# Optimization experiments

Measured on AMD Instinct MI355X. Metric: run time of the kernel, lower is better.

Reference implementation:

```python
import jax, jax.numpy as jnp
import numpy as np

VOCAB = 50257
C = 8  # n_dim_categories
B, T = 4, 4096


def setup_inputs() -> dict:
    key = jax.random.key(0)
    k1, k2, k3 = jax.random.split(key, 3)
    token_ids = jax.random.randint(k1, (B, T), 0, VOCAB)
    dim_embedding = jax.random.normal(k2, (VOCAB, C), dtype=jnp.float32)
    compatibility = jax.random.normal(k3, (C, C), dtype=jnp.float32) * 0.1
    return {"token_ids": token_ids, "dim_embedding": dim_embedding,
            "compatibility": compatibility}


def reference(token_ids, dim_embedding, compatibility):
    # (B,T,C): embedding lookup then softmax over categories
    dim_probs = jax.nn.softmax(dim_embedding[token_ids], axis=-1)
    # bilinear compatibility over all T x T token pairs -> (B,T,T)
    compat = jnp.einsum('btc,cd,bsd->bts', dim_probs, compatibility, dim_probs)
    mask_bias = jax.nn.sigmoid(compat) * 2 - 1
    return mask_bias
```

## Files before the change

kernel.cpp:

```cpp
#include <hip/hip_runtime.h>
#include <hip/hip_bf16.h>

typedef float f32x4 __attribute__((ext_vector_type(4)));

namespace {
constexpr int kB = 4;
constexpr int kT = 4096;
constexpr int kC = 8;
constexpr int kTRows = 64;
constexpr int kSPerThread = 4;
constexpr int kBlockThreads = 256;
constexpr int kWaves = kBlockThreads / 64;
constexpr int kSTile = kBlockThreads * kSPerThread;
}

__device__ __forceinline__ void softmax8_nomax(const float e[kC], float p[kC]) {
    float sum = 0.f;
#pragma unroll
    for (int i = 0; i < kC; ++i) { p[i] = __expf(e[i]); sum += p[i]; }
    float inv = __builtin_amdgcn_rcpf(sum);
#pragma unroll
    for (int i = 0; i < kC; ++i) p[i] *= inv;
}

__global__ __launch_bounds__(256) void dam_fused(const int* __restrict__ token_ids,
                                                 const float* __restrict__ emb,
                                                 const float* __restrict__ cmat,
                                                 float* __restrict__ out) {
    const int b = blockIdx.z;
    const int t0 = blockIdx.y * kTRows;
    const int s0 = blockIdx.x * kSTile;
    const int tid = threadIdx.x;
    const int wid = tid >> 6;
    const int lane = tid & 63;

    __shared__ f32x4 w_lds[kWaves][kTRows * 2];

    int tokT = token_ids[b * kT + t0 + lane];
    const f32x4* prow = reinterpret_cast<const f32x4*>(emb) + (size_t)tokT * 2;
    f32x4 pe0 = prow[0], pe1 = prow[1];

    const int s = s0 + tid * kSPerThread;
    int4 toks = *reinterpret_cast<const int4*>(&token_ids[b * kT + s]);
    int tokS[kSPerThread] = {toks.x, toks.y, toks.z, toks.w};
    f32x4 se[kSPerThread][2];
#pragma unroll
    for (int j = 0; j < kSPerThread; ++j) {
        const f32x4* srow = reinterpret_cast<const f32x4*>(emb) + (size_t)tokS[j] * 2;
        se[j][0] = srow[0];
        se[j][1] = srow[1];
    }

    {
        float e[kC] = {pe0.x, pe0.y, pe0.z, pe0.w, pe1.x, pe1.y, pe1.z, pe1.w};
        float p[kC];
        softmax8_nomax(e, p);
        float w[kC];
#pragma unroll
        for (int c = 0; c < kC; ++c) {
            float acc = 0.f;
#pragma unroll
            for (int d = 0; d < kC; ++d) acc = fmaf(cmat[d * kC + c], p[d], acc);
            w[c] = -acc;
        }
        w_lds[wid][lane * 2 + 0] = f32x4{w[0], w[1], w[2], w[3]};
        w_lds[wid][lane * 2 + 1] = f32x4{w[4], w[5], w[6], w[7]};
    }

    float q[kSPerThread][kC];
#pragma unroll
    for (int j = 0; j < kSPerThread; ++j) {
        float e[kC] = {se[j][0].x, se[j][0].y, se[j][0].z, se[j][0].w,
                       se[j][1].x, se[j][1].y, se[j][1].z, se[j][1].w};
        softmax8_nomax(e, q[j]);
    }

    float* orow = out + ((size_t)(b * kT + t0)) * kT + s;
#pragma unroll 4
    for (int tt = 0; tt < kTRows; ++tt) {
        f32x4 w0 = w_lds[wid][tt * 2 + 0];
        f32x4 w1 = w_lds[wid][tt * 2 + 1];
        float wr[kC] = {w0.x, w0.y, w0.z, w0.w, w1.x, w1.y, w1.z, w1.w};
        float r[kSPerThread];
#pragma unroll
        for (int j = 0; j < kSPerThread; ++j) {
            float acc = 0.f;
#pragma unroll
            for (int i = 0; i < kC; ++i) acc = fmaf(wr[i], q[j][i], acc);
            float ex = __expf(acc);
            r[j] = (1.f - ex) * __builtin_amdgcn_rcpf(1.f + ex);
        }
        f32x4 ov = {r[0], r[1], r[2], r[3]};
        *reinterpret_cast<f32x4*>(orow + (size_t)tt * kT) = ov;
    }
}

extern "C" void kernel_launch(void* const* d_in, const int* in_sizes, int n_in,
                              void* d_out, int out_size, void* d_ws, size_t ws_size,
                              hipStream_t stream) {
    const int* token_ids = (const int*)d_in[0];
    const float* emb     = (const float*)d_in[1];
    const float* cmat    = (const float*)d_in[2];
    float* out = (float*)d_out;

    dim3 grid(kT / kSTile, kT / kTRows, kB);
    dam_fused<<<grid, kBlockThreads, 0, stream>>>(token_ids, emb, cmat, out);
}
```

Measured before the change: 49.66 us.

## Precompute per-token softmax probabilities in a separate prep kernel

Splits the fused kernel into a prep kernel that gathers each token's embedding row and computes its softmax once into workspace, and a mask kernel that reads the precomputed probabilities contiguously. This removes the redundant gather and softmax that every block repeated for its T and S tokens, and turns random embedding gathers into coalesced reads. It adds a second launch and a small workspace round trip. The main kernel is bound by the large output write, so the saving may be small next to the extra launch.

After: 52.69 us. +6.1%, slower.

```diff
diff --git a/kernel.cpp b/kernel.cpp
--- a/kernel.cpp
+++ b/kernel.cpp
@@ -7,6 +7,7 @@
 constexpr int kB = 4;
 constexpr int kT = 4096;
 constexpr int kC = 8;
+constexpr int kN = kB * kT;
 constexpr int kTRows = 64;
 constexpr int kSPerThread = 4;
 constexpr int kBlockThreads = 256;
@@ -23,10 +24,24 @@
     for (int i = 0; i < kC; ++i) p[i] *= inv;
 }
 
-__global__ __launch_bounds__(256) void dam_fused(const int* __restrict__ token_ids,
-                                                 const float* __restrict__ emb,
-                                                 const float* __restrict__ cmat,
-                                                 float* __restrict__ out) {
+__global__ __launch_bounds__(64) void dam_prep(const int* __restrict__ token_ids,
+                                               const float* __restrict__ emb,
+                                               float* __restrict__ q_ws) {
+    const int i = blockIdx.x * 64 + threadIdx.x;
+    const int tok = token_ids[i];
+    const f32x4* row = reinterpret_cast<const f32x4*>(emb) + (size_t)tok * 2;
+    f32x4 e0 = row[0], e1 = row[1];
+    float e[kC] = {e0.x, e0.y, e0.z, e0.w, e1.x, e1.y, e1.z, e1.w};
+    float q[kC];
+    softmax8_nomax(e, q);
+    f32x4* qo = reinterpret_cast<f32x4*>(q_ws) + (size_t)i * 2;
+    qo[0] = f32x4{q[0], q[1], q[2], q[3]};
+    qo[1] = f32x4{q[4], q[5], q[6], q[7]};
+}
+
+__global__ __launch_bounds__(256) void dam_mask(const float* __restrict__ q_ws,
+                                                const float* __restrict__ cmat,
+                                                float* __restrict__ out) {
     const int b = blockIdx.z;
     const int t0 = blockIdx.y * kTRows;
     const int s0 = blockIdx.x * kSTile;
@@ -36,25 +51,18 @@
 
     __shared__ f32x4 w_lds[kWaves][kTRows * 2];
 
-    int tokT = token_ids[b * kT + t0 + lane];
-    const f32x4* prow = reinterpret_cast<const f32x4*>(emb) + (size_t)tokT * 2;
-    f32x4 pe0 = prow[0], pe1 = prow[1];
+    const f32x4* qt = reinterpret_cast<const f32x4*>(q_ws) + ((size_t)(b * kT + t0)) * 2;
+    f32x4 pe0 = qt[lane * 2 + 0];
+    f32x4 pe1 = qt[lane * 2 + 1];
 
     const int s = s0 + tid * kSPerThread;
-    int4 toks = *reinterpret_cast<const int4*>(&token_ids[b * kT + s]);
-    int tokS[kSPerThread] = {toks.x, toks.y, toks.z, toks.w};
-    f32x4 se[kSPerThread][2];
+    const f32x4* qs = reinterpret_cast<const f32x4*>(q_ws) + ((size_t)(b * kT) + s) * 2;
+    f32x4 se[kSPerThread * 2];
 #pragma unroll
-    for (int j = 0; j < kSPerThread; ++j) {
-        const f32x4* srow = reinterpret_cast<const f32x4*>(emb) + (size_t)tokS[j] * 2;
-        se[j][0] = srow[0];
-        se[j][1] = srow[1];
-    }
+    for (int k = 0; k < kSPerThread * 2; ++k) se[k] = qs[k];
 
     {
-        float e[kC] = {pe0.x, pe0.y, pe0.z, pe0.w, pe1.x, pe1.y, pe1.z, pe1.w};
-        float p[kC];
-        softmax8_nomax(e, p);
+        float p[kC] = {pe0.x, pe0.y, pe0.z, pe0.w, pe1.x, pe1.y, pe1.z, pe1.w};
         float w[kC];
 #pragma unroll
         for (int c = 0; c < kC; ++c) {
@@ -70,9 +78,10 @@
     float q[kSPerThread][kC];
 #pragma unroll
     for (int j = 0; j < kSPerThread; ++j) {
-        float e[kC] = {se[j][0].x, se[j][0].y, se[j][0].z, se[j][0].w,
-                       se[j][1].x, se[j][1].y, se[j][1].z, se[j][1].w};
-        softmax8_nomax(e, q[j]);
+        f32x4 a = se[j * 2 + 0];
+        f32x4 c = se[j * 2 + 1];
+        q[j][0] = a.x; q[j][1] = a.y; q[j][2] = a.z; q[j][3] = a.w;
+        q[j][4] = c.x; q[j][5] = c.y; q[j][6] = c.z; q[j][7] = c.w;
     }
 
     float* orow = out + ((size_t)(b * kT + t0)) * kT + s;
@@ -101,8 +110,10 @@
     const int* token_ids = (const int*)d_in[0];
     const float* emb     = (const float*)d_in[1];
     const float* cmat    = (const float*)d_in[2];
-    float* out = (float*)d_out;
+    float* out  = (float*)d_out;
+    float* q_ws = (float*)d_ws;
 
+    dam_prep<<<kN / 64, 64, 0, stream>>>(token_ids, emb, q_ws);
     dim3 grid(kT / kSTile, kT / kTRows, kB);
-    dam_fused<<<grid, kBlockThreads, 0, stream>>>(token_ids, emb, cmat, out);
+    dam_mask<<<grid, kBlockThreads, 0, stream>>>(q_ws, cmat, out);
 }
```
